# Performance work log

Measured on AMD Instinct MI355X. Metric: run time of the kernel, lower is better.

The kernel has to match this reference:

```python
import jax, jax.numpy as jnp
import numpy as np

CUTOFF = 5.0
NUM_RADIAL = 8
MAX_DEGREE = 3
NUM_EMB = 64
N_ELEM = 83
N_ATOMS = 20000
N_NBR = 32

# degree index for each of the 16 (l,m) components: l=0(x1),1(x3),2(x5),3(x7)
_LM_TO_L = np.repeat(np.arange(MAX_DEGREE + 1), [1, 3, 5, 7])


def jinclike(x, num, limit):
    """Jinc-like radial basis, f_n version (arXiv:1907.02374). x: (...,) -> (..., num)."""
    i = jnp.arange(num, dtype=jnp.float32)
    factor1 = (2.0 ** 0.5) * jnp.pi / (limit ** 1.5)
    factor2 = ((-1.0) ** i) * (i + 1.0) * (i + 2.0) / jnp.hypot(i + 1.0, i + 2.0)
    x = x[..., None]
    return factor1 * factor2 * (jnp.sinc(x / limit * (i + 1.0)) + jnp.sinc(x / limit * (i + 2.0)))


def sph_harm16(u):
    """Real spherical harmonics up to l=3, Racah normalization (Y00=1),
    spherical order m=-l..l (cartesian_order=False). u: (..., 3) unit vectors -> (..., 16)."""
    x, y, z = u[..., 0], u[..., 1], u[..., 2]
    s3, s6, s10, s15 = 3.0 ** 0.5, 6.0 ** 0.5, 10.0 ** 0.5, 15.0 ** 0.5
    one = jnp.ones_like(x)
    comps = [
        one,                                   # l=0
        y, z, x,                               # l=1, m=-1,0,1
        s3 * x * y, s3 * y * z, 0.5 * (3.0 * z * z - 1.0), s3 * x * z, 0.5 * s3 * (x * x - y * y),  # l=2
        0.25 * s10 * y * (3.0 * x * x - y * y), s15 * x * y * z, 0.25 * s6 * y * (5.0 * z * z - 1.0),
        0.5 * z * (5.0 * z * z - 3.0),
        0.25 * s6 * x * (5.0 * z * z - 1.0), 0.5 * s15 * z * (x * x - y * y), 0.25 * s10 * x * (x * x - 3.0 * y * y),  # l=3
    ]
    return jnp.stack(comps, axis=-1)


def setup_inputs() -> dict:
    key = jax.random.key(0)
    k1, k2, k3, k4, k5, k6 = jax.random.split(key, 6)
    neighbour_displacements = 1.5 * jax.random.normal(k1, (N_ATOMS, N_NBR, 3), dtype=jnp.float32)
    Z_j = jax.random.randint(k2, (N_ATOMS, N_NBR), 0, N_ELEM, dtype=jnp.int32)
    embed_table = jax.random.normal(k3, (N_ELEM, NUM_EMB), dtype=jnp.float32)
    dense_w = jax.random.normal(k4, (NUM_EMB, NUM_RADIAL), dtype=jnp.float32) / (NUM_EMB ** 0.5)
    dense_b = 0.01 * jax.random.normal(k5, (NUM_RADIAL,), dtype=jnp.float32)
    tensor_w = jax.random.normal(k6, (MAX_DEGREE + 1, NUM_RADIAL), dtype=jnp.float32)
    return {"neighbour_displacements": neighbour_displacements, "Z_j": Z_j,
            "embed_table": embed_table, "dense_w": dense_w, "dense_b": dense_b,
            "tensor_w": tensor_w}


def reference(neighbour_displacements, Z_j, embed_table, dense_w, dense_b, tensor_w):
    # radial x angular basis expansion: (N, K, 16, 8)
    norm = jnp.linalg.norm(neighbour_displacements, axis=-1)            # (N, K)
    u = neighbour_displacements / norm[..., None]                        # unit vectors
    rbf = jinclike(norm, NUM_RADIAL, CUTOFF)                             # (N, K, 8)
    sh = sph_harm16(u)                                                   # (N, K, 16)
    basis = sh[..., :, None] * rbf[..., None, :]                         # (N, K, 16, 8)

    # species embedding -> dense transform to num_radial channels (scalar, l=0 features)
    emb = embed_table[Z_j]                                               # (N, K, 64)
    t = emb @ dense_w + dense_b                                          # (N, K, 8)

    # CG tensor product with a scalar (l=0) left input collapses exactly to a
    # per-degree weighted elementwise product: y[lm,f] = w[l(lm),f] * t[f] * basis[lm,f]
    wexp = tensor_w[_LM_TO_L]                                            # (16, 8)
    y = wexp * t[..., None, :] * basis                                   # (N, K, 16, 8)

    y = y.at[..., 0, :].add(t)

    return y[..., None, :, :].astype(jnp.float32)
```

## Files before the change

### kernel.cpp

```cpp
#include <hip/hip_runtime.h>
#include <math.h>

#define N_ATOMS   20000
#define N_NBR     32
#define NBR_TOTAL (N_ATOMS * N_NBR)
#define N_ELEM    83
#define NUM_EMB   64
#define ROWW      34

typedef float f32x4 __attribute__((ext_vector_type(4)));

__global__ __launch_bounds__(256) void f_table_kernel(
    const float* __restrict__ embed, const float* __restrict__ dw,
    const float* __restrict__ db, float* __restrict__ F)
{
    const int i = blockIdx.x * 256 + threadIdx.x;
    if (i < N_ELEM * 8) {
        const int z = i >> 3, f = i & 7;
        float acc = db[f];
        const float* er = embed + z * NUM_EMB;
        #pragma unroll 8
        for (int e = 0; e < NUM_EMB; ++e)
            acc = fmaf(er[e], dw[e * 8 + f], acc);
        F[i] = acc;
    }
}

__global__ __launch_bounds__(256) void sarb_kernel(
    const float* __restrict__ disp,
    const int*   __restrict__ Zj,
    const float* __restrict__ tw,
    const float* __restrict__ Fg,
    float* __restrict__ out)
{
    __shared__ float Fl[N_ELEM * 9 + 1];
    __shared__ __align__(16) float lds[256 * ROWW];

    const int tid = threadIdx.x;

    for (int i = tid; i < N_ELEM * 8; i += 256)
        Fl[(i >> 3) * 9 + (i & 7)] = Fg[i];
    __syncthreads();

    const int n = blockIdx.x * 256 + tid;
    const float dx = disp[3 * n + 0];
    const float dy = disp[3 * n + 1];
    const float dz = disp[3 * n + 2];
    const int   z  = Zj[n];

    const float r2  = dx * dx + dy * dy + dz * dz;
    const float nrm = sqrtf(r2);
    const float inv = 1.0f / nrm;
    const float x = dx * inv, y = dy * inv, zu = dz * inv;

    const float s3 = 1.7320508075688772f, s6 = 2.449489742783178f;
    const float s10 = 3.1622776601683795f, s15 = 3.872983346207417f;
    const float x2 = x * x, y2 = y * y, z2 = zu * zu;
    const float xy = x * y, yz = y * zu, xz = x * zu;

    float* row = lds + tid * ROWW;
    row[0]  = 1.0f;
    row[1]  = y;
    row[2]  = zu;
    row[3]  = x;
    row[4]  = s3 * xy;
    row[5]  = s3 * yz;
    row[6]  = 0.5f * (3.0f * z2 - 1.0f);
    row[7]  = s3 * xz;
    row[8]  = 0.5f * s3 * (x2 - y2);
    row[9]  = 0.25f * s10 * y * (3.0f * x2 - y2);
    row[10] = s15 * xy * zu;
    row[11] = 0.25f * s6 * y * (5.0f * z2 - 1.0f);
    row[12] = 0.5f * zu * (5.0f * z2 - 3.0f);
    row[13] = 0.25f * s6 * x * (5.0f * z2 - 1.0f);
    row[14] = 0.5f * s15 * zu * (x2 - y2);
    row[15] = 0.25f * s10 * x * (x2 - 3.0f * y2);

    const float a = 0.6283185307179586f * nrm;
    float sv[9];
    {
        float s1, c1;
        __sincosf(a, &s1, &c1);
        const float c2   = 2.0f * c1;
        const float inva = 1.0f / a;
        const float invk[9] = {1.0f, 0.5f, 0.33333334f, 0.25f, 0.2f,
                               0.16666667f, 0.14285715f, 0.125f, 0.11111111f};
        float sprev = 0.0f, scur = s1;
        #pragma unroll
        for (int k = 0; k < 9; ++k) {
            sv[k] = scur * inva * invk[k];
            const float snext = c2 * scur - sprev;
            sprev = scur; scur = snext;
        }
        if (a < 1e-12f) {
            #pragma unroll
            for (int k = 0; k < 9; ++k) sv[k] = 1.0f;
        }
    }
    #pragma unroll
    for (int i = 0; i < 8; ++i) {
        const float ip1 = (float)(i + 1), ip2 = (float)(i + 2);
        float f2 = ip1 * ip2 / sqrtf(ip1 * ip1 + ip2 * ip2);
        if (i & 1) f2 = -f2;
        const float rbf = 0.3973835397f * f2 * (sv[i] + sv[i + 1]);
        const float tf  = Fl[z * 9 + i];
        row[16 + i] = tf * rbf;
        row[24 + i] = fmaf(tw[i] * rbf, tf, tf);
    }
    __syncthreads();

    const int chunk = tid & 31;
    const int lm  = chunk >> 1;
    const int fh4 = chunk & 1;
    const int l   = (lm > 0) + (lm > 3) + (lm > 8);
    f32x4 wv;
    if (lm == 0) { wv = (f32x4){1.0f, 1.0f, 1.0f, 1.0f}; }
    else         { wv = *reinterpret_cast<const f32x4*>(tw + l * 8 + fh4 * 4); }
    const int goff = (lm ? 16 : 24) + fh4 * 4;

    f32x4* __restrict__ outv =
        reinterpret_cast<f32x4*>(out) + (size_t)blockIdx.x * 8192;
    const int nb0 = tid >> 5;
    #pragma unroll
    for (int k = 0; k < 32; ++k) {
        const int rb = (k * 8 + nb0) * ROWW;
        const float  s  = lds[rb + lm];
        const float2 ga = *reinterpret_cast<const float2*>(lds + rb + goff);
        const float2 gb = *reinterpret_cast<const float2*>(lds + rb + goff + 2);
        f32x4 r;
        r.x = wv.x * s * ga.x;
        r.y = wv.y * s * ga.y;
        r.z = wv.z * s * gb.x;
        r.w = wv.w * s * gb.y;
        __builtin_nontemporal_store(r, outv + k * 256 + tid);
    }
}

extern "C" void kernel_launch(void* const* d_in, const int* in_sizes, int n_in,
                              void* d_out, int out_size, void* d_ws, size_t ws_size,
                              hipStream_t stream) {
    const float* disp  = (const float*)d_in[0];
    const int*   Zj    = (const int*)  d_in[1];
    const float* embed = (const float*)d_in[2];
    const float* dw    = (const float*)d_in[3];
    const float* db    = (const float*)d_in[4];
    const float* tw    = (const float*)d_in[5];
    float* out = (float*)d_out;
    float* F   = (float*)d_ws;

    f_table_kernel<<<dim3(3), dim3(256), 0, stream>>>(embed, dw, db, F);
    sarb_kernel<<<dim3(NBR_TOTAL / 256), dim3(256), 0, stream>>>(disp, Zj, tw, F, out);
}
```

Baseline: 344.8 us.

## Persistent wave-level tiling with per-wave LDS transpose and no block barriers

Replaces the one-tile-per-block launch with a persistent grid of 1024 blocks, where each wave independently loops over 64-neighbour tiles and uses only its own LDS region, so no __syncthreads is needed. The species table is read straight from global memory instead of being staged into LDS per block, LDS rows are written as 16-byte vectors with padding of 36, and stores become plain instead of nontemporal. The aim is to remove block-wide barriers and per-block setup cost while keeping output writes coalesced. The trade-off is correctness resting on wave-synchronous LDS behaviour enforced through inline waitcnt and sched barriers, and the possible loss of nontemporal store benefits.

```diff
diff --git a/kernel.cpp b/kernel.cpp
--- a/kernel.cpp
+++ b/kernel.cpp
@@ -4,9 +4,13 @@
 #define N_ATOMS   20000
 #define N_NBR     32
 #define NBR_TOTAL (N_ATOMS * N_NBR)
+#define N_TILES   (NBR_TOTAL / 64)
 #define N_ELEM    83
 #define NUM_EMB   64
-#define ROWW      34
+#define ROWF      36
+#define NBLK      1024
+#define NTHR      256
+#define WAVES_TOTAL (NBLK * NTHR / 64)
 
 typedef float f32x4 __attribute__((ext_vector_type(4)));
 
@@ -33,106 +37,121 @@
     const float* __restrict__ Fg,
     float* __restrict__ out)
 {
-    __shared__ float Fl[N_ELEM * 9 + 1];
-    __shared__ __align__(16) float lds[256 * ROWW];
+    __shared__ __align__(16) float lds[4 * 64 * ROWF];
 
-    const int tid = threadIdx.x;
+    const int tid  = threadIdx.x;
+    const int lane = tid & 63;
+    const int wib  = tid >> 6;
+    const int gw   = blockIdx.x * 4 + wib;
+    float* __restrict__ wlds = lds + wib * 64 * ROWF;
 
-    for (int i = tid; i < N_ELEM * 8; i += 256)
-        Fl[(i >> 3) * 9 + (i & 7)] = Fg[i];
-    __syncthreads();
-
-    const int n = blockIdx.x * 256 + tid;
-    const float dx = disp[3 * n + 0];
-    const float dy = disp[3 * n + 1];
-    const float dz = disp[3 * n + 2];
-    const int   z  = Zj[n];
-
-    const float r2  = dx * dx + dy * dy + dz * dz;
-    const float nrm = sqrtf(r2);
-    const float inv = 1.0f / nrm;
-    const float x = dx * inv, y = dy * inv, zu = dz * inv;
-
-    const float s3 = 1.7320508075688772f, s6 = 2.449489742783178f;
-    const float s10 = 3.1622776601683795f, s15 = 3.872983346207417f;
-    const float x2 = x * x, y2 = y * y, z2 = zu * zu;
-    const float xy = x * y, yz = y * zu, xz = x * zu;
-
-    float* row = lds + tid * ROWW;
-    row[0]  = 1.0f;
-    row[1]  = y;
-    row[2]  = zu;
-    row[3]  = x;
-    row[4]  = s3 * xy;
-    row[5]  = s3 * yz;
-    row[6]  = 0.5f * (3.0f * z2 - 1.0f);
-    row[7]  = s3 * xz;
-    row[8]  = 0.5f * s3 * (x2 - y2);
-    row[9]  = 0.25f * s10 * y * (3.0f * x2 - y2);
-    row[10] = s15 * xy * zu;
-    row[11] = 0.25f * s6 * y * (5.0f * z2 - 1.0f);
-    row[12] = 0.5f * zu * (5.0f * z2 - 3.0f);
-    row[13] = 0.25f * s6 * x * (5.0f * z2 - 1.0f);
-    row[14] = 0.5f * s15 * zu * (x2 - y2);
-    row[15] = 0.25f * s10 * x * (x2 - 3.0f * y2);
-
-    const float a = 0.6283185307179586f * nrm;
-    float sv[9];
-    {
-        float s1, c1;
-        __sincosf(a, &s1, &c1);
-        const float c2   = 2.0f * c1;
-        const float inva = 1.0f / a;
-        const float invk[9] = {1.0f, 0.5f, 0.33333334f, 0.25f, 0.2f,
-                               0.16666667f, 0.14285715f, 0.125f, 0.11111111f};
-        float sprev = 0.0f, scur = s1;
-        #pragma unroll
-        for (int k = 0; k < 9; ++k) {
-            sv[k] = scur * inva * invk[k];
-            const float snext = c2 * scur - sprev;
-            sprev = scur; scur = snext;
-        }
-        if (a < 1e-12f) {
-            #pragma unroll
-            for (int k = 0; k < 9; ++k) sv[k] = 1.0f;
-        }
-    }
-    #pragma unroll
-    for (int i = 0; i < 8; ++i) {
-        const float ip1 = (float)(i + 1), ip2 = (float)(i + 2);
-        float f2 = ip1 * ip2 / sqrtf(ip1 * ip1 + ip2 * ip2);
-        if (i & 1) f2 = -f2;
-        const float rbf = 0.3973835397f * f2 * (sv[i] + sv[i + 1]);
-        const float tf  = Fl[z * 9 + i];
-        row[16 + i] = tf * rbf;
-        row[24 + i] = fmaf(tw[i] * rbf, tf, tf);
-    }
-    __syncthreads();
-
-    const int chunk = tid & 31;
-    const int lm  = chunk >> 1;
-    const int fh4 = chunk & 1;
+    const int c   = lane & 31;
+    const int lm  = c >> 1;
+    const int fh4 = c & 1;
+    const int hi  = lane >> 5;
     const int l   = (lm > 0) + (lm > 3) + (lm > 8);
     f32x4 wv;
     if (lm == 0) { wv = (f32x4){1.0f, 1.0f, 1.0f, 1.0f}; }
     else         { wv = *reinterpret_cast<const f32x4*>(tw + l * 8 + fh4 * 4); }
     const int goff = (lm ? 16 : 24) + fh4 * 4;
+    const float* __restrict__ rd_s = wlds + hi * ROWF + lm;
+    const float* __restrict__ rd_g = wlds + hi * ROWF + goff;
 
-    f32x4* __restrict__ outv =
-        reinterpret_cast<f32x4*>(out) + (size_t)blockIdx.x * 8192;
-    const int nb0 = tid >> 5;
+    float twv[8], Fv[8];
     #pragma unroll
-    for (int k = 0; k < 32; ++k) {
-        const int rb = (k * 8 + nb0) * ROWW;
-        const float  s  = lds[rb + lm];
-        const float2 ga = *reinterpret_cast<const float2*>(lds + rb + goff);
-        const float2 gb = *reinterpret_cast<const float2*>(lds + rb + goff + 2);
-        f32x4 r;
-        r.x = wv.x * s * ga.x;
-        r.y = wv.y * s * ga.y;
-        r.z = wv.z * s * gb.x;
-        r.w = wv.w * s * gb.y;
-        __builtin_nontemporal_store(r, outv + k * 256 + tid);
+    for (int i = 0; i < 8; ++i) twv[i] = tw[i];
+
+    const int t0 = (int)(((long long)gw       * N_TILES) / WAVES_TOTAL);
+    const int t1 = (int)(((long long)(gw + 1) * N_TILES) / WAVES_TOTAL);
+
+    for (int t = t0; t < t1; ++t) {
+        const int n = (t << 6) + lane;
+        const float dx = disp[3 * n + 0];
+        const float dy = disp[3 * n + 1];
+        const float dz = disp[3 * n + 2];
+        const int   z  = Zj[n];
+
+        const float nrm = sqrtf(dx * dx + dy * dy + dz * dz);
+        const float inv = 1.0f / nrm;
+        const float x = dx * inv, y = dy * inv, zu = dz * inv;
+
+        const float s3 = 1.7320508075688772f, s6 = 2.449489742783178f;
+        const float s10 = 3.1622776601683795f, s15 = 3.872983346207417f;
+        const float x2 = x * x, y2 = y * y, z2 = zu * zu;
+        const float xy = x * y, yz = y * zu, xz = x * zu;
+
+        const f32x4 sA = {1.0f, y, zu, x};
+        const f32x4 sB = {s3 * xy, s3 * yz, 0.5f * (3.0f * z2 - 1.0f), s3 * xz};
+        const f32x4 sC = {0.5f * s3 * (x2 - y2), 0.25f * s10 * y * (3.0f * x2 - y2),
+                          s15 * xy * zu, 0.25f * s6 * y * (5.0f * z2 - 1.0f)};
+        const f32x4 sD = {0.5f * zu * (5.0f * z2 - 3.0f), 0.25f * s6 * x * (5.0f * z2 - 1.0f),
+                          0.5f * s15 * zu * (x2 - y2), 0.25f * s10 * x * (x2 - 3.0f * y2)};
+
+        const float a = 0.6283185307179586f * nrm;
+        float sv[9];
+        {
+            float s1, c1;
+            __sincosf(a, &s1, &c1);
+            const float c2   = 2.0f * c1;
+            const float inva = 1.0f / a;
+            const float invk[9] = {1.0f, 0.5f, 0.33333334f, 0.25f, 0.2f,
+                                   0.16666667f, 0.14285715f, 0.125f, 0.11111111f};
+            float sprev = 0.0f, scur = s1;
+            #pragma unroll
+            for (int k = 0; k < 9; ++k) {
+                sv[k] = scur * inva * invk[k];
+                const float snext = c2 * scur - sprev;
+                sprev = scur; scur = snext;
+            }
+            if (a < 1e-12f) {
+                #pragma unroll
+                for (int k = 0; k < 9; ++k) sv[k] = 1.0f;
+            }
+        }
+
+        *reinterpret_cast<f32x4*>(Fv)     = *reinterpret_cast<const f32x4*>(Fg + z * 8);
+        *reinterpret_cast<f32x4*>(Fv + 4) = *reinterpret_cast<const f32x4*>(Fg + z * 8 + 4);
+
+        float gv[8], hv[8];
+        #pragma unroll
+        for (int i = 0; i < 8; ++i) {
+            const float ip1 = (float)(i + 1), ip2 = (float)(i + 2);
+            float f2 = ip1 * ip2 / sqrtf(ip1 * ip1 + ip2 * ip2);
+            if (i & 1) f2 = -f2;
+            const float rbf = 0.3973835397f * f2 * (sv[i] + sv[i + 1]);
+            const float tf  = Fv[i];
+            gv[i] = tf * rbf;
+            hv[i] = fmaf(twv[i] * rbf, tf, tf);
+        }
+
+        float* __restrict__ rowp = wlds + lane * ROWF;
+        *reinterpret_cast<f32x4*>(rowp +  0) = sA;
+        *reinterpret_cast<f32x4*>(rowp +  4) = sB;
+        *reinterpret_cast<f32x4*>(rowp +  8) = sC;
+        *reinterpret_cast<f32x4*>(rowp + 12) = sD;
+        *reinterpret_cast<f32x4*>(rowp + 16) = (f32x4){gv[0], gv[1], gv[2], gv[3]};
+        *reinterpret_cast<f32x4*>(rowp + 20) = (f32x4){gv[4], gv[5], gv[6], gv[7]};
+        *reinterpret_cast<f32x4*>(rowp + 24) = (f32x4){hv[0], hv[1], hv[2], hv[3]};
+        *reinterpret_cast<f32x4*>(rowp + 28) = (f32x4){hv[4], hv[5], hv[6], hv[7]};
+
+        asm volatile("s_waitcnt lgkmcnt(0)" ::: "memory");
+        __builtin_amdgcn_sched_barrier(0);
+
+        f32x4* __restrict__ outv = reinterpret_cast<f32x4*>(out) + (size_t)t * 2048 + lane;
+        #pragma unroll
+        for (int k = 0; k < 32; ++k) {
+            const float s = rd_s[k * 2 * ROWF];
+            const f32x4 g = *reinterpret_cast<const f32x4*>(rd_g + k * 2 * ROWF);
+            f32x4 r;
+            r.x = wv.x * s * g.x;
+            r.y = wv.y * s * g.y;
+            r.z = wv.z * s * g.z;
+            r.w = wv.w * s * g.w;
+            outv[k * 64] = r;
+        }
+
+        asm volatile("s_waitcnt lgkmcnt(0)" ::: "memory");
+        __builtin_amdgcn_sched_barrier(0);
     }
 }
 
@@ -149,5 +168,5 @@
     float* F   = (float*)d_ws;
 
     f_table_kernel<<<dim3(3), dim3(256), 0, stream>>>(embed, dw, db, F);
-    sarb_kernel<<<dim3(NBR_TOTAL / 256), dim3(256), 0, stream>>>(disp, Zj, tw, F, out);
+    sarb_kernel<<<dim3(NBLK), dim3(NTHR), 0, stream>>>(disp, Zj, tw, F, out);
 }
```

Result: no change. 350.2 us (+1.6%).
